# Kernel optimization log

Hardware: AMD Instinct MI355X
Metric: run time of the kernel (lower is better)

## Reference

```python
import jax, jax.numpy as jnp
import numpy as np

B, H, S, D = 4, 16, 2048, 64
TEMPERATURE = 8.0  # sqrt(D)
NEG = -1000000000.0

def setup_inputs() -> dict:
    key = jax.random.key(0)
    kq, kk, kv, km = jax.random.split(key, 4)
    q = jax.random.normal(kq, (B, H, S, D), dtype=jnp.float32)
    k = jax.random.normal(kk, (B, H, S, D), dtype=jnp.float32)
    v = jax.random.normal(kv, (B, H, S, D), dtype=jnp.float32)
    mask = jax.random.randint(km, (B, 1, S, S), 0, 2, dtype=jnp.int32)
    return {"q": q, "k": k, "v": v, "mask": mask}

def reference(q, k, v, mask):
    # scores: [B,H,S,S]
    scores = jnp.einsum('bhqd,bhkd->bhqk', q / TEMPERATURE, k)
    scores = jnp.where(mask == 1, NEG, scores)
    attn = jax.nn.softmax(scores, axis=-1)  # dropout p=0.0 -> identity
    out = jnp.einsum('bhqk,bhkd->bhqd', attn, v)
    return out
```

## Files before the change

kernel.cpp:

```cpp
#include <hip/hip_runtime.h>

#define NB 4
#define NH 16
#define SS 2048
#define DD 64
#define QT 256
#define KT 64
#define NT (SS / KT)
#define KSP 72
#define QSCALE 0.18033688011112042f

#define WS_BITS_BYTES ((size_t)NB * SS * (SS / 8))
#define WS_KB_OFF  ((size_t)2  << 20)
#define WS_VB_OFF  ((size_t)18 << 20)
#define WS_FULL    ((size_t)34 << 20)

typedef __bf16 bf16x8 __attribute__((ext_vector_type(8)));
typedef __bf16 bf16x2 __attribute__((ext_vector_type(2)));
typedef float  floatx16 __attribute__((ext_vector_type(16)));
typedef unsigned long long u64t;

static_assert(sizeof(bf16x8) == 16, "bf16x8 must be 16B");

__device__ __forceinline__ int pack2(float a, float b) {
    bf16x2 v; v[0] = (__bf16)a; v[1] = (__bf16)b;
    return __builtin_bit_cast(int, v);
}

__device__ __forceinline__ int vperm_col(int k) {
    return 16 * (k >> 4) + 8 * ((k >> 2) & 1) + (k & 3) + 4 * ((k >> 3) & 1);
}
__device__ __forceinline__ int vperm_inv(int c) {
    return 16 * ((c >> 4) & 3) + 8 * ((c >> 2) & 1) + 4 * ((c >> 3) & 1) + (c & 3);
}

__global__ __launch_bounds__(256)
void pack_mask_kernel(const int* __restrict__ M, u64t* __restrict__ bits)
{
    const int w    = (blockIdx.x * 256 + threadIdx.x) >> 6;
    const int lane = threadIdx.x & 63;
    #pragma unroll 4
    for (int i = 0; i < 16; ++i) {
        const int gw   = i * 16384 + w;
        const size_t row = (size_t)(gw >> 5);
        const int word = gw & 31;
        const int mval = M[row * SS + (size_t)word * 64 + lane];
        const u64t b = __ballot(mval == 1);
        if (lane == 0) bits[gw] = b;
    }
}

__global__ __launch_bounds__(256)
void pre_kernel(const float* __restrict__ K, const float* __restrict__ V,
                const int* __restrict__ M, u64t* __restrict__ bits,
                __bf16* __restrict__ KB, __bf16* __restrict__ VB)
{
    __shared__ float vt[64][68];
    const int t = threadIdx.x;

    if (blockIdx.x < 2048) {
        const int bh = blockIdx.x >> 5;
        const int tt = blockIdx.x & 31;
        const size_t tb = (size_t)bh * SS * DD + (size_t)tt * (KT * DD);

        {
            const float* src = K + tb + t * 16;
            __bf16* dst = KB + tb + t * 16;
            float4 f0 = ((const float4*)src)[0];
            float4 f1 = ((const float4*)src)[1];
            float4 f2 = ((const float4*)src)[2];
            float4 f3 = ((const float4*)src)[3];
            bf16x8 o0, o1;
            o0[0]=(__bf16)f0.x; o0[1]=(__bf16)f0.y; o0[2]=(__bf16)f0.z; o0[3]=(__bf16)f0.w;
            o0[4]=(__bf16)f1.x; o0[5]=(__bf16)f1.y; o0[6]=(__bf16)f1.z; o0[7]=(__bf16)f1.w;
            o1[0]=(__bf16)f2.x; o1[1]=(__bf16)f2.y; o1[2]=(__bf16)f2.z; o1[3]=(__bf16)f2.w;
            o1[4]=(__bf16)f3.x; o1[5]=(__bf16)f3.y; o1[6]=(__bf16)f3.z; o1[7]=(__bf16)f3.w;
            ((bf16x8*)dst)[0] = o0;
            ((bf16x8*)dst)[1] = o1;
        }

        {
            const int key = t >> 2, ds = (t & 3) * 16;
            const float* src = V + tb + (size_t)key * DD + ds;
            #pragma unroll
            for (int i = 0; i < 4; ++i)
                *(float4*)&vt[key][ds + 4 * i] = ((const float4*)src)[i];
        }
        __syncthreads();
        {
            const int dim = t >> 2, cb = (t & 3) * 16;
            bf16x8 o0, o1;
            #pragma unroll
            for (int c = 0; c < 16; ++c) {
                const float vvv = vt[vperm_inv(cb + c)][dim];
                if (c < 8) o0[c] = (__bf16)vvv; else o1[c - 8] = (__bf16)vvv;
            }
            __bf16* dst = VB + tb + (size_t)dim * 64 + cb;
            ((bf16x8*)dst)[0] = o0;
            ((bf16x8*)dst)[1] = o1;
        }
    } else {
        const int w    = ((blockIdx.x - 2048) * 256 + t) >> 6;
        const int lane = t & 63;
        #pragma unroll 4
        for (int i = 0; i < 16; ++i) {
            const int gw   = i * 16384 + w;
            const size_t row = (size_t)(gw >> 5);
            const int word = gw & 31;
            const int mval = M[row * SS + (size_t)word * 64 + lane];
            const u64t b = __ballot(mval == 1);
            if (lane == 0) bits[gw] = b;
        }
    }
}

__global__ __launch_bounds__(256, 2)
void attn2_kernel(const float* __restrict__ Q, const unsigned* __restrict__ MBu,
                  const __bf16* __restrict__ KB, const __bf16* __restrict__ VB,
                  float* __restrict__ O)
{
    __shared__ __bf16 ks [2][KT][KSP];
    __shared__ __bf16 vsT[2][DD][KSP];

    const int t    = threadIdx.x;
    const int lane = t & 63;
    const int l31  = lane & 31;
    const int h8   = lane >> 5;
    const int wave = t >> 6;

    const int bh    = blockIdx.x & 63;
    const int qtile = blockIdx.x >> 6;
    const int b     = bh >> 4;
    const int q0    = qtile * QT + wave * 64;

    const size_t base = (size_t)bh * SS * DD;

    bf16x8 aqA[4], aqB[4];
    #pragma unroll
    for (int grp = 0; grp < 2; ++grp) {
        const float* qp = Q + base + (size_t)(q0 + 32 * grp + l31) * DD + 8 * h8;
        #pragma unroll
        for (int s = 0; s < 4; ++s) {
            float4 f0 = *(const float4*)(qp + 16 * s);
            float4 f1 = *(const float4*)(qp + 16 * s + 4);
            bf16x8 a;
            a[0] = (__bf16)(f0.x * QSCALE); a[1] = (__bf16)(f0.y * QSCALE);
            a[2] = (__bf16)(f0.z * QSCALE); a[3] = (__bf16)(f0.w * QSCALE);
            a[4] = (__bf16)(f1.x * QSCALE); a[5] = (__bf16)(f1.y * QSCALE);
            a[6] = (__bf16)(f1.z * QSCALE); a[7] = (__bf16)(f1.w * QSCALE);
            if (grp == 0) aqA[s] = a; else aqB[s] = a;
        }
    }

    const int srow = t >> 3;
    const int sc8  = (t & 7) * 8;
    const __bf16* kbp = KB + base + (size_t)srow * DD + sc8;
    const __bf16* vbp = VB + base + (size_t)srow * DD + sc8;
    bf16x8 kr0, kr1, vr0, vr1;

    kr0 = *(const bf16x8*)kbp;
    kr1 = *(const bf16x8*)(kbp + 32 * DD);
    vr0 = *(const bf16x8*)vbp;
    vr1 = *(const bf16x8*)(vbp + 32 * DD);

    const u64t* mbrA = (const u64t*)MBu + ((size_t)b * SS + q0 + l31)      * (SS / 64);
    const u64t* mbrB = (const u64t*)MBu + ((size_t)b * SS + q0 + 32 + l31) * (SS / 64);
    u64t mA = mbrA[0], mB = mbrB[0], mnA, mnB;

    floatx16 o0A, o1A, o0B, o1B;
    #pragma unroll
    for (int i = 0; i < 16; ++i) {
        o0A[i] = 0.f; o1A[i] = 0.f; o0B[i] = 0.f; o1B[i] = 0.f;
    }
    float lsA = 0.f, lsB = 0.f;

    for (int tt = 0; tt < NT; ++tt) {
        const int cur = tt & 1;

        *(bf16x8*)&ks [cur][srow]     [sc8] = kr0;
        *(bf16x8*)&ks [cur][srow + 32][sc8] = kr1;
        *(bf16x8*)&vsT[cur][srow]     [sc8] = vr0;
        *(bf16x8*)&vsT[cur][srow + 32][sc8] = vr1;

        asm volatile("s_waitcnt lgkmcnt(0)" ::: "memory");
        __builtin_amdgcn_s_barrier();
        asm volatile("" ::: "memory");

        {
            const size_t jn = (size_t)((tt + 1) & (NT - 1)) * (KT * DD);
            kr0 = *(const bf16x8*)(kbp + jn);
            kr1 = *(const bf16x8*)(kbp + jn + 32 * DD);
            vr0 = *(const bf16x8*)(vbp + jn);
            vr1 = *(const bf16x8*)(vbp + jn + 32 * DD);
        }
        mnA = mbrA[(tt + 1) & (NT - 1)];
        mnB = mbrB[(tt + 1) & (NT - 1)];

        __builtin_amdgcn_s_setprio(1);

        bf16x8 kf0[4], kf1[4];
        #pragma unroll
        for (int s = 0; s < 4; ++s) {
            kf0[s] = *(const bf16x8*)&ks[cur][l31]     [16 * s + 8 * h8];
            kf1[s] = *(const bf16x8*)&ks[cur][32 + l31][16 * s + 8 * h8];
        }

        floatx16 cA0, cB0, cA1, cB1;
        {
            const unsigned uA0 = (unsigned)(mA)       >> (4 * h8);
            const unsigned uB0 = (unsigned)(mB)       >> (4 * h8);
            const unsigned uA1 = (unsigned)(mA >> 32) >> (4 * h8);
            const unsigned uB1 = (unsigned)(mB >> 32) >> (4 * h8);
            #pragma unroll
            for (int i = 0; i < 16; ++i) {
                const int pos = (i & 3) + 8 * (i >> 2);
                cA0[i] = __builtin_bit_cast(float, (((int)(uA0 << (31 - pos))) >> 31) & (int)0xC4800000u);
                cB0[i] = __builtin_bit_cast(float, (((int)(uB0 << (31 - pos))) >> 31) & (int)0xC4800000u);
                cA1[i] = __builtin_bit_cast(float, (((int)(uA1 << (31 - pos))) >> 31) & (int)0xC4800000u);
                cB1[i] = __builtin_bit_cast(float, (((int)(uB1 << (31 - pos))) >> 31) & (int)0xC4800000u);
            }
        }

        #pragma unroll
        for (int s = 0; s < 4; ++s) {
            cA0 = __builtin_amdgcn_mfma_f32_32x32x16_bf16(kf0[s], aqA[s], cA0, 0, 0, 0);
            cB0 = __builtin_amdgcn_mfma_f32_32x32x16_bf16(kf0[s], aqB[s], cB0, 0, 0, 0);
            cA1 = __builtin_amdgcn_mfma_f32_32x32x16_bf16(kf1[s], aqA[s], cA1, 0, 0, 0);
            cB1 = __builtin_amdgcn_mfma_f32_32x32x16_bf16(kf1[s], aqB[s], cB1, 0, 0, 0);
        }

        int pkA0[8], pkB0[8];
        {
            float sa0 = 0.f, sa1 = 0.f, sb0 = 0.f, sb1 = 0.f;
            #pragma unroll
            for (int g = 0; g < 8; ++g) {
                float a0 = __builtin_amdgcn_exp2f(cA0[2 * g]);
                float a1 = __builtin_amdgcn_exp2f(cA0[2 * g + 1]);
                float b0 = __builtin_amdgcn_exp2f(cB0[2 * g]);
                float b1 = __builtin_amdgcn_exp2f(cB0[2 * g + 1]);
                sa0 += a0; sa1 += a1; sb0 += b0; sb1 += b1;
                pkA0[g] = pack2(a0, a1);
                pkB0[g] = pack2(b0, b1);
            }
            lsA += sa0 + sa1; lsB += sb0 + sb1;
        }

        #pragma unroll
        for (int s2 = 0; s2 < 2; ++s2) {
            bf16x8 av0 = *(const bf16x8*)&vsT[cur][l31]     [16 * s2 + 8 * h8];
            bf16x8 av1 = *(const bf16x8*)&vsT[cur][32 + l31][16 * s2 + 8 * h8];
            int4 fwA; fwA.x = pkA0[4*s2]; fwA.y = pkA0[4*s2+1]; fwA.z = pkA0[4*s2+2]; fwA.w = pkA0[4*s2+3];
            int4 fwB; fwB.x = pkB0[4*s2]; fwB.y = pkB0[4*s2+1]; fwB.z = pkB0[4*s2+2]; fwB.w = pkB0[4*s2+3];
            bf16x8 bpA = __builtin_bit_cast(bf16x8, fwA);
            bf16x8 bpB = __builtin_bit_cast(bf16x8, fwB);
            o0A = __builtin_amdgcn_mfma_f32_32x32x16_bf16(av0, bpA, o0A, 0, 0, 0);
            o0B = __builtin_amdgcn_mfma_f32_32x32x16_bf16(av0, bpB, o0B, 0, 0, 0);
            o1A = __builtin_amdgcn_mfma_f32_32x32x16_bf16(av1, bpA, o1A, 0, 0, 0);
            o1B = __builtin_amdgcn_mfma_f32_32x32x16_bf16(av1, bpB, o1B, 0, 0, 0);
        }

        int pkA1[8], pkB1[8];
        {
            float sa0 = 0.f, sa1 = 0.f, sb0 = 0.f, sb1 = 0.f;
            #pragma unroll
            for (int g = 0; g < 8; ++g) {
                float a0 = __builtin_amdgcn_exp2f(cA1[2 * g]);
                float a1 = __builtin_amdgcn_exp2f(cA1[2 * g + 1]);
                float b0 = __builtin_amdgcn_exp2f(cB1[2 * g]);
                float b1 = __builtin_amdgcn_exp2f(cB1[2 * g + 1]);
                sa0 += a0; sa1 += a1; sb0 += b0; sb1 += b1;
                pkA1[g] = pack2(a0, a1);
                pkB1[g] = pack2(b0, b1);
            }
            lsA += sa0 + sa1; lsB += sb0 + sb1;
        }

        #pragma unroll
        for (int s2 = 0; s2 < 2; ++s2) {
            bf16x8 av0 = *(const bf16x8*)&vsT[cur][l31]     [32 + 16 * s2 + 8 * h8];
            bf16x8 av1 = *(const bf16x8*)&vsT[cur][32 + l31][32 + 16 * s2 + 8 * h8];
            int4 fwA; fwA.x = pkA1[4*s2]; fwA.y = pkA1[4*s2+1]; fwA.z = pkA1[4*s2+2]; fwA.w = pkA1[4*s2+3];
            int4 fwB; fwB.x = pkB1[4*s2]; fwB.y = pkB1[4*s2+1]; fwB.z = pkB1[4*s2+2]; fwB.w = pkB1[4*s2+3];
            bf16x8 bpA = __builtin_bit_cast(bf16x8, fwA);
            bf16x8 bpB = __builtin_bit_cast(bf16x8, fwB);
            o0A = __builtin_amdgcn_mfma_f32_32x32x16_bf16(av0, bpA, o0A, 0, 0, 0);
            o0B = __builtin_amdgcn_mfma_f32_32x32x16_bf16(av0, bpB, o0B, 0, 0, 0);
            o1A = __builtin_amdgcn_mfma_f32_32x32x16_bf16(av1, bpA, o1A, 0, 0, 0);
            o1B = __builtin_amdgcn_mfma_f32_32x32x16_bf16(av1, bpB, o1B, 0, 0, 0);
        }

        __builtin_amdgcn_s_setprio(0);

        mA = mnA; mB = mnB;
    }

    lsA += __shfl_xor(lsA, 32);
    lsB += __shfl_xor(lsB, 32);
    const float invA = 1.0f / lsA;
    const float invB = 1.0f / lsB;
    float* opA = O + base + (size_t)(q0 + l31) * DD;
    float* opB = O + base + (size_t)(q0 + 32 + l31) * DD;
    #pragma unroll
    for (int s = 0; s < 4; ++s) {
        float4 st;
        st.x = o0A[4*s+0] * invA; st.y = o0A[4*s+1] * invA;
        st.z = o0A[4*s+2] * invA; st.w = o0A[4*s+3] * invA;
        *(float4*)(opA + 8 * s + 4 * h8) = st;
        st.x = o1A[4*s+0] * invA; st.y = o1A[4*s+1] * invA;
        st.z = o1A[4*s+2] * invA; st.w = o1A[4*s+3] * invA;
        *(float4*)(opA + 32 + 8 * s + 4 * h8) = st;
        st.x = o0B[4*s+0] * invB; st.y = o0B[4*s+1] * invB;
        st.z = o0B[4*s+2] * invB; st.w = o0B[4*s+3] * invB;
        *(float4*)(opB + 8 * s + 4 * h8) = st;
        st.x = o1B[4*s+0] * invB; st.y = o1B[4*s+1] * invB;
        st.z = o1B[4*s+2] * invB; st.w = o1B[4*s+3] * invB;
        *(float4*)(opB + 32 + 8 * s + 4 * h8) = st;
    }
}

template<int MODE>
__global__ __launch_bounds__(512, 4)
void attn_kernel(const float* __restrict__ Q, const float* __restrict__ K,
                 const float* __restrict__ V, const int* __restrict__ M,
                 const unsigned* __restrict__ MB, float* __restrict__ O)
{
    __shared__ __bf16 ks [2][KT][KSP];
    __shared__ __bf16 vsT[2][DD][KSP];

    const int t    = threadIdx.x;
    const int wave = t >> 6;
    const int lane = t & 63;
    const int l31  = lane & 31;
    const int h8   = lane >> 5;

    const int bh    = blockIdx.x & 63;
    const int qtile = blockIdx.x >> 6;
    const int b     = bh >> 4;
    const int q0    = qtile * QT + wave * 32;

    const size_t base = (size_t)bh * SS * DD;

    bf16x8 aq[4];
    {
        const float* qp = Q + base + (size_t)(q0 + l31) * DD + 8 * h8;
        #pragma unroll
        for (int s = 0; s < 4; ++s) {
            float4 f0 = *(const float4*)(qp + 16 * s);
            float4 f1 = *(const float4*)(qp + 16 * s + 4);
            bf16x8 a;
            a[0] = (__bf16)(f0.x * QSCALE); a[1] = (__bf16)(f0.y * QSCALE);
            a[2] = (__bf16)(f0.z * QSCALE); a[3] = (__bf16)(f0.w * QSCALE);
            a[4] = (__bf16)(f1.x * QSCALE); a[5] = (__bf16)(f1.y * QSCALE);
            a[6] = (__bf16)(f1.z * QSCALE); a[7] = (__bf16)(f1.w * QSCALE);
            aq[s] = a;
        }
    }

    bf16x8 ones8;
    #pragma unroll
    for (int i = 0; i < 8; ++i) ones8[i] = (__bf16)1.0f;

    const int skey = t >> 3;
    const int sdc  = (t & 7) * 8;
    const int vk   = 2 * (t & 31);
    const int vdc  = (t >> 5) * 4;
    const int vcol = vperm_col(vk);
    const float* kp0 = K + base + (size_t)skey * DD + sdc;
    const float* vp0 = V + base + (size_t)vk * DD + vdc;

    float4 ka0 = ((const float4*)kp0)[0];
    float4 ka1 = ((const float4*)kp0)[1];
    float4 va0 = *(const float4*)(vp0);
    float4 va1 = *(const float4*)(vp0 + DD);

    const u64t* mbrow = (const u64t*)MB + ((size_t)b * SS + q0 + l31) * (SS / 64);
    const int*  mrow  = M + (size_t)b * SS * SS + (size_t)(q0 + l31) * SS + 4 * h8;
    u64t mall = 0, mnext = 0;
    if constexpr (MODE >= 1) mall = mbrow[0];

    floatx16 o0, o1, oL;
    #pragma unroll
    for (int i = 0; i < 16; ++i) { o0[i] = 0.f; o1[i] = 0.f; oL[i] = 0.f; }

    for (int tt = 0; tt < NT; ++tt) {
        const int cur = tt & 1;

        {
            bf16x8 kw;
            kw[0]=(__bf16)ka0.x; kw[1]=(__bf16)ka0.y; kw[2]=(__bf16)ka0.z; kw[3]=(__bf16)ka0.w;
            kw[4]=(__bf16)ka1.x; kw[5]=(__bf16)ka1.y; kw[6]=(__bf16)ka1.z; kw[7]=(__bf16)ka1.w;
            *(bf16x8*)&ks[cur][skey][sdc] = kw;
            #pragma unroll
            for (int i = 0; i < 4; ++i) {
                bf16x2 pr;
                pr[0] = (__bf16)(&va0.x)[i]; pr[1] = (__bf16)(&va1.x)[i];
                *(bf16x2*)&vsT[cur][vdc + i][vcol] = pr;
            }
        }
        __syncthreads();

        int4 mi[8];
        if constexpr (MODE == 0) {
            #pragma unroll
            for (int g = 0; g < 8; ++g)
                mi[g] = *(const int4*)(mrow + tt * KT + 8 * g);
        }

        {
            const int jn = ((tt + 1) * KT) & (SS - 1);
            const float* kn = kp0 + (size_t)jn * DD;
            ka0 = ((const float4*)kn)[0];
            ka1 = ((const float4*)kn)[1];
            const float* vn = vp0 + (size_t)jn * DD;
            va0 = *(const float4*)(vn);
            va1 = *(const float4*)(vn + DD);
        }
        if constexpr (MODE >= 1) mnext = mbrow[(tt + 1) & (NT - 1)];

        #pragma unroll
        for (int half = 0; half < 2; ++half) {
            floatx16 c;
            if constexpr (MODE >= 1) {
                const unsigned u = (unsigned)(mall >> (32 * half)) >> (4 * h8);
                #pragma unroll
                for (int i = 0; i < 16; ++i) {
                    const int pos = (i & 3) + 8 * (i >> 2);
                    const int sm = ((int)(u << (31 - pos))) >> 31;
                    c[i] = __builtin_bit_cast(float, sm & (int)0xC4800000u);
                }
            } else {
                #pragma unroll
                for (int i = 0; i < 16; ++i) {
                    const int g2 = 4 * half + (i >> 2);
                    c[i] = ((&mi[g2].x)[i & 3] == 1) ? -1024.0f : 0.0f;
                }
            }

            __builtin_amdgcn_s_setprio(1);
            #pragma unroll
            for (int s = 0; s < 4; ++s) {
                bf16x8 a = *(const bf16x8*)&ks[cur][32 * half + l31][16 * s + 8 * h8];
                c = __builtin_amdgcn_mfma_f32_32x32x16_bf16(a, aq[s], c, 0, 0, 0);
            }
            __builtin_amdgcn_s_setprio(0);

            int pk[8];
            #pragma unroll
            for (int g = 0; g < 8; ++g) {
                float pa = __builtin_amdgcn_exp2f(c[2 * g]);
                float pb = __builtin_amdgcn_exp2f(c[2 * g + 1]);
                pk[g] = pack2(pa, pb);
            }

            __builtin_amdgcn_s_setprio(1);
            #pragma unroll
            for (int s2 = 0; s2 < 2; ++s2) {
                int4 fw; fw.x = pk[4*s2]; fw.y = pk[4*s2+1]; fw.z = pk[4*s2+2]; fw.w = pk[4*s2+3];
                bf16x8 bp = __builtin_bit_cast(bf16x8, fw);
                bf16x8 av0 = *(const bf16x8*)&vsT[cur][l31]     [32 * half + 16 * s2 + 8 * h8];
                bf16x8 av1 = *(const bf16x8*)&vsT[cur][32 + l31][32 * half + 16 * s2 + 8 * h8];
                o0 = __builtin_amdgcn_mfma_f32_32x32x16_bf16(av0, bp, o0, 0, 0, 0);
                o1 = __builtin_amdgcn_mfma_f32_32x32x16_bf16(av1, bp, o1, 0, 0, 0);
                oL = __builtin_amdgcn_mfma_f32_32x32x16_bf16(ones8, bp, oL, 0, 0, 0);
            }
            __builtin_amdgcn_s_setprio(0);
        }

        if constexpr (MODE >= 1) mall = mnext;
    }

    float inv = 1.0f / oL[0];
    float* op = O + base + (size_t)(q0 + l31) * DD;
    #pragma unroll
    for (int s = 0; s < 4; ++s) {
        float4 st0, st1;
        st0.x = o0[4*s+0] * inv; st0.y = o0[4*s+1] * inv;
        st0.z = o0[4*s+2] * inv; st0.w = o0[4*s+3] * inv;
        st1.x = o1[4*s+0] * inv; st1.y = o1[4*s+1] * inv;
        st1.z = o1[4*s+2] * inv; st1.w = o1[4*s+3] * inv;
        *(float4*)(op + 8 * s + 4 * h8)      = st0;
        *(float4*)(op + 32 + 8 * s + 4 * h8) = st1;
    }
}

extern "C" void kernel_launch(void* const* d_in, const int* in_sizes, int n_in,
                              void* d_out, int out_size, void* d_ws, size_t ws_size,
                              hipStream_t stream) {
    (void)in_sizes; (void)n_in; (void)out_size;
    const float* q = (const float*)d_in[0];
    const float* k = (const float*)d_in[1];
    const float* v = (const float*)d_in[2];
    const int*   m = (const int*)d_in[3];
    float* out = (float*)d_out;
    dim3 grid(NB * NH * (SS / QT));

    if (ws_size >= WS_FULL) {
        u64t*   bits = (u64t*)d_ws;
        __bf16* kb16 = (__bf16*)((char*)d_ws + WS_KB_OFF);
        __bf16* vb16 = (__bf16*)((char*)d_ws + WS_VB_OFF);
        pre_kernel<<<dim3(6144), 256, 0, stream>>>(k, v, m, bits, kb16, vb16);
        attn2_kernel<<<grid, 256, 0, stream>>>(q, (const unsigned*)bits,
                                               kb16, vb16, out);
    } else if (ws_size >= WS_BITS_BYTES) {
        u64t* bits = (u64t*)d_ws;
        pack_mask_kernel<<<dim3(4096), 256, 0, stream>>>(m, bits);
        attn_kernel<1><<<grid, 512, 0, stream>>>(q, k, v, m, (const unsigned*)bits, out);
    } else {
        attn_kernel<0><<<grid, 512, 0, stream>>>(q, k, v, m, nullptr, out);
    }
}
```

Baseline: 270.1 us.

## Pre-swizzle K/V into MFMA fragment order and load directly to registers, dropping LDS

```diff
diff --git a/kernel.cpp b/kernel.cpp
--- a/kernel.cpp
+++ b/kernel.cpp
@@ -55,7 +55,7 @@
                 const int* __restrict__ M, u64t* __restrict__ bits,
                 __bf16* __restrict__ KB, __bf16* __restrict__ VB)
 {
-    __shared__ float vt[64][68];
+    __shared__ float ft[64][68];
     const int t = threadIdx.x;
 
     if (blockIdx.x < 2048) {
@@ -64,40 +64,49 @@
         const size_t tb = (size_t)bh * SS * DD + (size_t)tt * (KT * DD);
 
         {
-            const float* src = K + tb + t * 16;
-            __bf16* dst = KB + tb + t * 16;
-            float4 f0 = ((const float4*)src)[0];
-            float4 f1 = ((const float4*)src)[1];
-            float4 f2 = ((const float4*)src)[2];
-            float4 f3 = ((const float4*)src)[3];
-            bf16x8 o0, o1;
-            o0[0]=(__bf16)f0.x; o0[1]=(__bf16)f0.y; o0[2]=(__bf16)f0.z; o0[3]=(__bf16)f0.w;
-            o0[4]=(__bf16)f1.x; o0[5]=(__bf16)f1.y; o0[6]=(__bf16)f1.z; o0[7]=(__bf16)f1.w;
-            o1[0]=(__bf16)f2.x; o1[1]=(__bf16)f2.y; o1[2]=(__bf16)f2.z; o1[3]=(__bf16)f2.w;
-            o1[4]=(__bf16)f3.x; o1[5]=(__bf16)f3.y; o1[6]=(__bf16)f3.z; o1[7]=(__bf16)f3.w;
-            ((bf16x8*)dst)[0] = o0;
-            ((bf16x8*)dst)[1] = o1;
-        }
+            const int key = t >> 2, ds = (t & 3) * 16;
+            const float* src = K + tb + (size_t)key * DD + ds;
+            #pragma unroll
+            for (int i = 0; i < 4; ++i)
+                *(float4*)&ft[key][ds + 4 * i] = ((const float4*)src)[i];
+        }
+        __syncthreads();
+        {
+            #pragma unroll
+            for (int rep = 0; rep < 2; ++rep) {
+                const int s = t + 256 * rep;
+                const int c = s >> 6, l = s & 63;
+                const int row = 32 * (c >> 2) + (l & 31);
+                const int col = 16 * (c & 3) + 8 * (l >> 5);
+                bf16x8 o;
+                #pragma unroll
+                for (int j = 0; j < 8; ++j) o[j] = (__bf16)ft[row][col + j];
+                *(bf16x8*)(KB + tb + (size_t)s * 8) = o;
+            }
+        }
+        __syncthreads();
 
         {
             const int key = t >> 2, ds = (t & 3) * 16;
             const float* src = V + tb + (size_t)key * DD + ds;
             #pragma unroll
             for (int i = 0; i < 4; ++i)
-                *(float4*)&vt[key][ds + 4 * i] = ((const float4*)src)[i];
+                *(float4*)&ft[key][ds + 4 * i] = ((const float4*)src)[i];
         }
         __syncthreads();
         {
-            const int dim = t >> 2, cb = (t & 3) * 16;
-            bf16x8 o0, o1;
-            #pragma unroll
-            for (int c = 0; c < 16; ++c) {
-                const float vvv = vt[vperm_inv(cb + c)][dim];
-                if (c < 8) o0[c] = (__bf16)vvv; else o1[c - 8] = (__bf16)vvv;
-            }
-            __bf16* dst = VB + tb + (size_t)dim * 64 + cb;
-            ((bf16x8*)dst)[0] = o0;
-            ((bf16x8*)dst)[1] = o1;
+            #pragma unroll
+            for (int rep = 0; rep < 2; ++rep) {
+                const int s = t + 256 * rep;
+                const int g = s >> 6, l = s & 63;
+                const int colb = 32 * (g >> 2) + 16 * ((g >> 1) & 1) + 8 * (l >> 5);
+                const int dim  = 32 * (g & 1) + (l & 31);
+                bf16x8 o;
+                #pragma unroll
+                for (int j = 0; j < 8; ++j)
+                    o[j] = (__bf16)ft[vperm_inv(colb + j)][dim];
+                *(bf16x8*)(VB + tb + (size_t)s * 8) = o;
+            }
         }
     } else {
         const int w    = ((blockIdx.x - 2048) * 256 + t) >> 6;
@@ -116,12 +125,9 @@
 
 __global__ __launch_bounds__(256, 2)
 void attn2_kernel(const float* __restrict__ Q, const unsigned* __restrict__ MBu,
-                  const __bf16* __restrict__ KB, const __bf16* __restrict__ VB,
+                  const __bf16* __restrict__ KBf, const __bf16* __restrict__ VBf,
                   float* __restrict__ O)
 {
-    __shared__ __bf16 ks [2][KT][KSP];
-    __shared__ __bf16 vsT[2][DD][KSP];
-
     const int t    = threadIdx.x;
     const int lane = t & 63;
     const int l31  = lane & 31;
@@ -152,20 +158,18 @@
         }
     }
 
-    const int srow = t >> 3;
-    const int sc8  = (t & 7) * 8;
-    const __bf16* kbp = KB + base + (size_t)srow * DD + sc8;
-    const __bf16* vbp = VB + base + (size_t)srow * DD + sc8;
-    bf16x8 kr0, kr1, vr0, vr1;
-
-    kr0 = *(const bf16x8*)kbp;
-    kr1 = *(const bf16x8*)(kbp + 32 * DD);
-    vr0 = *(const bf16x8*)vbp;
-    vr1 = *(const bf16x8*)(vbp + 32 * DD);
+    const __bf16* kfp = KBf + base + (size_t)lane * 8;
+    const __bf16* vfp = VBf + base + (size_t)lane * 8;
+
+    bf16x8 kf[8], vfr[8];
+    #pragma unroll
+    for (int g = 0; g < 8; ++g) kf[g]  = *(const bf16x8*)(kfp + g * 512);
+    #pragma unroll
+    for (int g = 0; g < 8; ++g) vfr[g] = *(const bf16x8*)(vfp + g * 512);
 
     const u64t* mbrA = (const u64t*)MBu + ((size_t)b * SS + q0 + l31)      * (SS / 64);
     const u64t* mbrB = (const u64t*)MBu + ((size_t)b * SS + q0 + 32 + l31) * (SS / 64);
-    u64t mA = mbrA[0], mB = mbrB[0], mnA, mnB;
+    u64t mA = mbrA[0], mB = mbrB[0];
 
     floatx16 o0A, o1A, o0B, o1B;
     #pragma unroll
@@ -175,35 +179,7 @@
     float lsA = 0.f, lsB = 0.f;
 
     for (int tt = 0; tt < NT; ++tt) {
-        const int cur = tt & 1;
-
-        *(bf16x8*)&ks [cur][srow]     [sc8] = kr0;
-        *(bf16x8*)&ks [cur][srow + 32][sc8] = kr1;
-        *(bf16x8*)&vsT[cur][srow]     [sc8] = vr0;
-        *(bf16x8*)&vsT[cur][srow + 32][sc8] = vr1;
-
-        asm volatile("s_waitcnt lgkmcnt(0)" ::: "memory");
-        __builtin_amdgcn_s_barrier();
-        asm volatile("" ::: "memory");
-
-        {
-            const size_t jn = (size_t)((tt + 1) & (NT - 1)) * (KT * DD);
-            kr0 = *(const bf16x8*)(kbp + jn);
-            kr1 = *(const bf16x8*)(kbp + jn + 32 * DD);
-            vr0 = *(const bf16x8*)(vbp + jn);
-            vr1 = *(const bf16x8*)(vbp + jn + 32 * DD);
-        }
-        mnA = mbrA[(tt + 1) & (NT - 1)];
-        mnB = mbrB[(tt + 1) & (NT - 1)];
-
-        __builtin_amdgcn_s_setprio(1);
-
-        bf16x8 kf0[4], kf1[4];
-        #pragma unroll
-        for (int s = 0; s < 4; ++s) {
-            kf0[s] = *(const bf16x8*)&ks[cur][l31]     [16 * s + 8 * h8];
-            kf1[s] = *(const bf16x8*)&ks[cur][32 + l31][16 * s + 8 * h8];
-        }
+        const size_t jn = (size_t)((tt + 1) & (NT - 1)) * (KT * DD);
 
         floatx16 cA0, cB0, cA1, cB1;
         {
@@ -220,14 +196,22 @@
                 cB1[i] = __builtin_bit_cast(float, (((int)(uB1 << (31 - pos))) >> 31) & (int)0xC4800000u);
             }
         }
-
+        mA = mbrA[(tt + 1) & (NT - 1)];
+        mB = mbrB[(tt + 1) & (NT - 1)];
+
+        __builtin_amdgcn_s_setprio(1);
         #pragma unroll
         for (int s = 0; s < 4; ++s) {
-            cA0 = __builtin_amdgcn_mfma_f32_32x32x16_bf16(kf0[s], aqA[s], cA0, 0, 0, 0);
-            cB0 = __builtin_amdgcn_mfma_f32_32x32x16_bf16(kf0[s], aqB[s], cB0, 0, 0, 0);
-            cA1 = __builtin_amdgcn_mfma_f32_32x32x16_bf16(kf1[s], aqA[s], cA1, 0, 0, 0);
-            cB1 = __builtin_amdgcn_mfma_f32_32x32x16_bf16(kf1[s], aqB[s], cB1, 0, 0, 0);
-        }
+            cA0 = __builtin_amdgcn_mfma_f32_32x32x16_bf16(kf[s],     aqA[s], cA0, 0, 0, 0);
+            cB0 = __builtin_amdgcn_mfma_f32_32x32x16_bf16(kf[s],     aqB[s], cB0, 0, 0, 0);
+            cA1 = __builtin_amdgcn_mfma_f32_32x32x16_bf16(kf[4 + s], aqA[s], cA1, 0, 0, 0);
+            cB1 = __builtin_amdgcn_mfma_f32_32x32x16_bf16(kf[4 + s], aqB[s], cB1, 0, 0, 0);
+        }
+        __builtin_amdgcn_s_setprio(0);
+
+        #pragma unroll
+        for (int g = 0; g < 8; ++g)
+            kf[g] = *(const bf16x8*)(kfp + jn + g * 512);
 
         int pkA0[8], pkB0[8];
         {
@@ -245,10 +229,11 @@
             lsA += sa0 + sa1; lsB += sb0 + sb1;
         }
 
+        __builtin_amdgcn_s_setprio(1);
         #pragma unroll
         for (int s2 = 0; s2 < 2; ++s2) {
-            bf16x8 av0 = *(const bf16x8*)&vsT[cur][l31]     [16 * s2 + 8 * h8];
-            bf16x8 av1 = *(const bf16x8*)&vsT[cur][32 + l31][16 * s2 + 8 * h8];
+            bf16x8 av0 = vfr[s2 * 2 + 0];
+            bf16x8 av1 = vfr[s2 * 2 + 1];
             int4 fwA; fwA.x = pkA0[4*s2]; fwA.y = pkA0[4*s2+1]; fwA.z = pkA0[4*s2+2]; fwA.w = pkA0[4*s2+3];
             int4 fwB; fwB.x = pkB0[4*s2]; fwB.y = pkB0[4*s2+1]; fwB.z = pkB0[4*s2+2]; fwB.w = pkB0[4*s2+3];
             bf16x8 bpA = __builtin_bit_cast(bf16x8, fwA);
@@ -258,6 +243,7 @@
             o1A = __builtin_amdgcn_mfma_f32_32x32x16_bf16(av1, bpA, o1A, 0, 0, 0);
             o1B = __builtin_amdgcn_mfma_f32_32x32x16_bf16(av1, bpB, o1B, 0, 0, 0);
         }
+        __builtin_amdgcn_s_setprio(0);
 
         int pkA1[8], pkB1[8];
         {
@@ -275,10 +261,11 @@
             lsA += sa0 + sa1; lsB += sb0 + sb1;
         }
 
+        __builtin_amdgcn_s_setprio(1);
         #pragma unroll
         for (int s2 = 0; s2 < 2; ++s2) {
-            bf16x8 av0 = *(const bf16x8*)&vsT[cur][l31]     [32 + 16 * s2 + 8 * h8];
-            bf16x8 av1 = *(const bf16x8*)&vsT[cur][32 + l31][32 + 16 * s2 + 8 * h8];
+            bf16x8 av0 = vfr[4 + s2 * 2 + 0];
+            bf16x8 av1 = vfr[4 + s2 * 2 + 1];
             int4 fwA; fwA.x = pkA1[4*s2]; fwA.y = pkA1[4*s2+1]; fwA.z = pkA1[4*s2+2]; fwA.w = pkA1[4*s2+3];
             int4 fwB; fwB.x = pkB1[4*s2]; fwB.y = pkB1[4*s2+1]; fwB.z = pkB1[4*s2+2]; fwB.w = pkB1[4*s2+3];
             bf16x8 bpA = __builtin_bit_cast(bf16x8, fwA);
@@ -288,10 +275,11 @@
             o1A = __builtin_amdgcn_mfma_f32_32x32x16_bf16(av1, bpA, o1A, 0, 0, 0);
             o1B = __builtin_amdgcn_mfma_f32_32x32x16_bf16(av1, bpB, o1B, 0, 0, 0);
         }
-
         __builtin_amdgcn_s_setprio(0);
 
-        mA = mnA; mB = mnB;
+        #pragma unroll
+        for (int g = 0; g < 8; ++g)
+            vfr[g] = *(const bf16x8*)(vfp + jn + g * 512);
     }
 
     lsA += __shfl_xor(lsA, 32);
```

New measurement: 303.6 us. +12.4%, slower.

## Double the key tile per barrier stage to 128 keys in attention kernel

Applied to the files above, without the earlier changes.

```diff
diff --git a/kernel.cpp b/kernel.cpp
--- a/kernel.cpp
+++ b/kernel.cpp
@@ -6,8 +6,10 @@
 #define DD 64
 #define QT 256
 #define KT 64
-#define NT (SS / KT)
+#define ST 128
+#define NST (SS / ST)
 #define KSP 72
+#define VSP 136
 #define QSCALE 0.18033688011112042f
 
 #define WS_BITS_BYTES ((size_t)NB * SS * (SS / 8))
@@ -119,8 +121,8 @@
                   const __bf16* __restrict__ KB, const __bf16* __restrict__ VB,
                   float* __restrict__ O)
 {
-    __shared__ __bf16 ks [2][KT][KSP];
-    __shared__ __bf16 vsT[2][DD][KSP];
+    __shared__ __bf16 ks [2][ST][KSP];
+    __shared__ __bf16 vsT[2][DD][VSP];
 
     const int t    = threadIdx.x;
     const int lane = t & 63;
@@ -156,16 +158,21 @@
     const int sc8  = (t & 7) * 8;
     const __bf16* kbp = KB + base + (size_t)srow * DD + sc8;
     const __bf16* vbp = VB + base + (size_t)srow * DD + sc8;
-    bf16x8 kr0, kr1, vr0, vr1;
-
-    kr0 = *(const bf16x8*)kbp;
-    kr1 = *(const bf16x8*)(kbp + 32 * DD);
-    vr0 = *(const bf16x8*)vbp;
-    vr1 = *(const bf16x8*)(vbp + 32 * DD);
+    bf16x8 kr[4], vr[4];
+
+    {
+        #pragma unroll
+        for (int i = 0; i < 4; ++i)
+            kr[i] = *(const bf16x8*)(kbp + (size_t)(32 * i) * DD);
+        vr[0] = *(const bf16x8*)(vbp);
+        vr[1] = *(const bf16x8*)(vbp + 32 * DD);
+        vr[2] = *(const bf16x8*)(vbp + KT * DD);
+        vr[3] = *(const bf16x8*)(vbp + KT * DD + 32 * DD);
+    }
 
     const u64t* mbrA = (const u64t*)MBu + ((size_t)b * SS + q0 + l31)      * (SS / 64);
     const u64t* mbrB = (const u64t*)MBu + ((size_t)b * SS + q0 + 32 + l31) * (SS / 64);
-    u64t mA = mbrA[0], mB = mbrB[0], mnA, mnB;
+    u64t mA0 = mbrA[0], mA1 = mbrA[1], mB0 = mbrB[0], mB1 = mbrB[1];
 
     floatx16 o0A, o1A, o0B, o1B;
     #pragma unroll
@@ -174,124 +181,139 @@
     }
     float lsA = 0.f, lsB = 0.f;
 
-    for (int tt = 0; tt < NT; ++tt) {
+    for (int tt = 0; tt < NST; ++tt) {
         const int cur = tt & 1;
 
-        *(bf16x8*)&ks [cur][srow]     [sc8] = kr0;
-        *(bf16x8*)&ks [cur][srow + 32][sc8] = kr1;
-        *(bf16x8*)&vsT[cur][srow]     [sc8] = vr0;
-        *(bf16x8*)&vsT[cur][srow + 32][sc8] = vr1;
+        #pragma unroll
+        for (int i = 0; i < 4; ++i)
+            *(bf16x8*)&ks[cur][srow + 32 * i][sc8] = kr[i];
+        *(bf16x8*)&vsT[cur][srow]     [sc8]      = vr[0];
+        *(bf16x8*)&vsT[cur][srow + 32][sc8]      = vr[1];
+        *(bf16x8*)&vsT[cur][srow]     [64 + sc8] = vr[2];
+        *(bf16x8*)&vsT[cur][srow + 32][64 + sc8] = vr[3];
 
         asm volatile("s_waitcnt lgkmcnt(0)" ::: "memory");
         __builtin_amdgcn_s_barrier();
         asm volatile("" ::: "memory");
 
         {
-            const size_t jn = (size_t)((tt + 1) & (NT - 1)) * (KT * DD);
-            kr0 = *(const bf16x8*)(kbp + jn);
-            kr1 = *(const bf16x8*)(kbp + jn + 32 * DD);
-            vr0 = *(const bf16x8*)(vbp + jn);
-            vr1 = *(const bf16x8*)(vbp + jn + 32 * DD);
-        }
-        mnA = mbrA[(tt + 1) & (NT - 1)];
-        mnB = mbrB[(tt + 1) & (NT - 1)];
-
-        __builtin_amdgcn_s_setprio(1);
-
-        bf16x8 kf0[4], kf1[4];
+            const size_t jn = (size_t)((tt + 1) & (NST - 1)) * (ST * DD);
+            #pragma unroll
+            for (int i = 0; i < 4; ++i)
+                kr[i] = *(const bf16x8*)(kbp + jn + (size_t)(32 * i) * DD);
+            vr[0] = *(const bf16x8*)(vbp + jn);
+            vr[1] = *(const bf16x8*)(vbp + jn + 32 * DD);
+            vr[2] = *(const bf16x8*)(vbp + jn + KT * DD);
+            vr[3] = *(const bf16x8*)(vbp + jn + KT * DD + 32 * DD);
+        }
+        const int nw = (2 * tt + 2) & (2 * NST - 1);
+        u64t nA0 = mbrA[nw], nA1 = mbrA[nw + 1];
+        u64t nB0 = mbrB[nw], nB1 = mbrB[nw + 1];
+
         #pragma unroll
-        for (int s = 0; s < 4; ++s) {
-            kf0[s] = *(const bf16x8*)&ks[cur][l31]     [16 * s + 8 * h8];
-            kf1[s] = *(const bf16x8*)&ks[cur][32 + l31][16 * s + 8 * h8];
-        }
-
-        floatx16 cA0, cB0, cA1, cB1;
-        {
-            const unsigned uA0 = (unsigned)(mA)       >> (4 * h8);
-            const unsigned uB0 = (unsigned)(mB)       >> (4 * h8);
-            const unsigned uA1 = (unsigned)(mA >> 32) >> (4 * h8);
-            const unsigned uB1 = (unsigned)(mB >> 32) >> (4 * h8);
-            #pragma unroll
-            for (int i = 0; i < 16; ++i) {
-                const int pos = (i & 3) + 8 * (i >> 2);
-                cA0[i] = __builtin_bit_cast(float, (((int)(uA0 << (31 - pos))) >> 31) & (int)0xC4800000u);
-                cB0[i] = __builtin_bit_cast(float, (((int)(uB0 << (31 - pos))) >> 31) & (int)0xC4800000u);
-                cA1[i] = __builtin_bit_cast(float, (((int)(uA1 << (31 - pos))) >> 31) & (int)0xC4800000u);
-                cB1[i] = __builtin_bit_cast(float, (((int)(uB1 << (31 - pos))) >> 31) & (int)0xC4800000u);
-            }
-        }
-
-        #pragma unroll
-        for (int s = 0; s < 4; ++s) {
-            cA0 = __builtin_amdgcn_mfma_f32_32x32x16_bf16(kf0[s], aqA[s], cA0, 0, 0, 0);
-            cB0 = __builtin_amdgcn_mfma_f32_32x32x16_bf16(kf0[s], aqB[s], cB0, 0, 0, 0);
-            cA1 = __builtin_amdgcn_mfma_f32_32x32x16_bf16(kf1[s], aqA[s], cA1, 0, 0, 0);
-            cB1 = __builtin_amdgcn_mfma_f32_32x32x16_bf16(kf1[s], aqB[s], cB1, 0, 0, 0);
-        }
-
-        int pkA0[8], pkB0[8];
-        {
-            float sa0 = 0.f, sa1 = 0.f, sb0 = 0.f, sb1 = 0.f;
-            #pragma unroll
-            for (int g = 0; g < 8; ++g) {
-                float a0 = __builtin_amdgcn_exp2f(cA0[2 * g]);
-                float a1 = __builtin_amdgcn_exp2f(cA0[2 * g + 1]);
-                float b0 = __builtin_amdgcn_exp2f(cB0[2 * g]);
-                float b1 = __builtin_amdgcn_exp2f(cB0[2 * g + 1]);
-                sa0 += a0; sa1 += a1; sb0 += b0; sb1 += b1;
-                pkA0[g] = pack2(a0, a1);
-                pkB0[g] = pack2(b0, b1);
-            }
-            lsA += sa0 + sa1; lsB += sb0 + sb1;
-        }
-
-        #pragma unroll
-        for (int s2 = 0; s2 < 2; ++s2) {
-            bf16x8 av0 = *(const bf16x8*)&vsT[cur][l31]     [16 * s2 + 8 * h8];
-            bf16x8 av1 = *(const bf16x8*)&vsT[cur][32 + l31][16 * s2 + 8 * h8];
-            int4 fwA; fwA.x = pkA0[4*s2]; fwA.y = pkA0[4*s2+1]; fwA.z = pkA0[4*s2+2]; fwA.w = pkA0[4*s2+3];
-            int4 fwB; fwB.x = pkB0[4*s2]; fwB.y = pkB0[4*s2+1]; fwB.z = pkB0[4*s2+2]; fwB.w = pkB0[4*s2+3];
-            bf16x8 bpA = __builtin_bit_cast(bf16x8, fwA);
-            bf16x8 bpB = __builtin_bit_cast(bf16x8, fwB);
-            o0A = __builtin_amdgcn_mfma_f32_32x32x16_bf16(av0, bpA, o0A, 0, 0, 0);
-            o0B = __builtin_amdgcn_mfma_f32_32x32x16_bf16(av0, bpB, o0B, 0, 0, 0);
-            o1A = __builtin_amdgcn_mfma_f32_32x32x16_bf16(av1, bpA, o1A, 0, 0, 0);
-            o1B = __builtin_amdgcn_mfma_f32_32x32x16_bf16(av1, bpB, o1B, 0, 0, 0);
-        }
-
-        int pkA1[8], pkB1[8];
-        {
-            float sa0 = 0.f, sa1 = 0.f, sb0 = 0.f, sb1 = 0.f;
-            #pragma unroll
-            for (int g = 0; g < 8; ++g) {
-                float a0 = __builtin_amdgcn_exp2f(cA1[2 * g]);
-                float a1 = __builtin_amdgcn_exp2f(cA1[2 * g + 1]);
-                float b0 = __builtin_amdgcn_exp2f(cB1[2 * g]);
-                float b1 = __builtin_amdgcn_exp2f(cB1[2 * g + 1]);
-                sa0 += a0; sa1 += a1; sb0 += b0; sb1 += b1;
-                pkA1[g] = pack2(a0, a1);
-                pkB1[g] = pack2(b0, b1);
-            }
-            lsA += sa0 + sa1; lsB += sb0 + sb1;
-        }
-
-        #pragma unroll
-        for (int s2 = 0; s2 < 2; ++s2) {
-            bf16x8 av0 = *(const bf16x8*)&vsT[cur][l31]     [32 + 16 * s2 + 8 * h8];
-            bf16x8 av1 = *(const bf16x8*)&vsT[cur][32 + l31][32 + 16 * s2 + 8 * h8];
-            int4 fwA; fwA.x = pkA1[4*s2]; fwA.y = pkA1[4*s2+1]; fwA.z = pkA1[4*s2+2]; fwA.w = pkA1[4*s2+3];
-            int4 fwB; fwB.x = pkB1[4*s2]; fwB.y = pkB1[4*s2+1]; fwB.z = pkB1[4*s2+2]; fwB.w = pkB1[4*s2+3];
-            bf16x8 bpA = __builtin_bit_cast(bf16x8, fwA);
-            bf16x8 bpB = __builtin_bit_cast(bf16x8, fwB);
-            o0A = __builtin_amdgcn_mfma_f32_32x32x16_bf16(av0, bpA, o0A, 0, 0, 0);
-            o0B = __builtin_amdgcn_mfma_f32_32x32x16_bf16(av0, bpB, o0B, 0, 0, 0);
-            o1A = __builtin_amdgcn_mfma_f32_32x32x16_bf16(av1, bpA, o1A, 0, 0, 0);
-            o1B = __builtin_amdgcn_mfma_f32_32x32x16_bf16(av1, bpB, o1B, 0, 0, 0);
-        }
-
-        __builtin_amdgcn_s_setprio(0);
-
-        mA = mnA; mB = mnB;
+        for (int hp = 0; hp < 2; ++hp) {
+            const u64t wA = hp ? mA1 : mA0;
+            const u64t wB = hp ? mB1 : mB0;
+
+            floatx16 cA0, cB0, cA1, cB1;
+            {
+                const unsigned uA0 = (unsigned)(wA)       >> (4 * h8);
+                const unsigned uB0 = (unsigned)(wB)       >> (4 * h8);
+                const unsigned uA1 = (unsigned)(wA >> 32) >> (4 * h8);
+                const unsigned uB1 = (unsigned)(wB >> 32) >> (4 * h8);
+                #pragma unroll
+                for (int i = 0; i < 16; ++i) {
+                    const int pos = (i & 3) + 8 * (i >> 2);
+                    cA0[i] = __builtin_bit_cast(float, (((int)(uA0 << (31 - pos))) >> 31) & (int)0xC4800000u);
+                    cB0[i] = __builtin_bit_cast(float, (((int)(uB0 << (31 - pos))) >> 31) & (int)0xC4800000u);
+                    cA1[i] = __builtin_bit_cast(float, (((int)(uA1 << (31 - pos))) >> 31) & (int)0xC4800000u);
+                    cB1[i] = __builtin_bit_cast(float, (((int)(uB1 << (31 - pos))) >> 31) & (int)0xC4800000u);
+                }
+            }
+
+            __builtin_amdgcn_s_setprio(1);
+            bf16x8 kf0[4], kf1[4];
+            #pragma unroll
+            for (int s = 0; s < 4; ++s) {
+                kf0[s] = *(const bf16x8*)&ks[cur][64 * hp + l31]     [16 * s + 8 * h8];
+                kf1[s] = *(const bf16x8*)&ks[cur][64 * hp + 32 + l31][16 * s + 8 * h8];
+            }
+
+            #pragma unroll
+            for (int s = 0; s < 4; ++s) {
+                cA0 = __builtin_amdgcn_mfma_f32_32x32x16_bf16(kf0[s], aqA[s], cA0, 0, 0, 0);
+                cB0 = __builtin_amdgcn_mfma_f32_32x32x16_bf16(kf0[s], aqB[s], cB0, 0, 0, 0);
+                cA1 = __builtin_amdgcn_mfma_f32_32x32x16_bf16(kf1[s], aqA[s], cA1, 0, 0, 0);
+                cB1 = __builtin_amdgcn_mfma_f32_32x32x16_bf16(kf1[s], aqB[s], cB1, 0, 0, 0);
+            }
+            __builtin_amdgcn_s_setprio(0);
+
+            int pkA0[8], pkB0[8];
+            {
+                float sa0 = 0.f, sa1 = 0.f, sb0 = 0.f, sb1 = 0.f;
+                #pragma unroll
+                for (int g = 0; g < 8; ++g) {
+                    float a0 = __builtin_amdgcn_exp2f(cA0[2 * g]);
+                    float a1 = __builtin_amdgcn_exp2f(cA0[2 * g + 1]);
+                    float b0 = __builtin_amdgcn_exp2f(cB0[2 * g]);
+                    float b1 = __builtin_amdgcn_exp2f(cB0[2 * g + 1]);
+                    sa0 += a0; sa1 += a1; sb0 += b0; sb1 += b1;
+                    pkA0[g] = pack2(a0, a1);
+                    pkB0[g] = pack2(b0, b1);
+                }
+                lsA += sa0 + sa1; lsB += sb0 + sb1;
+            }
+
+            __builtin_amdgcn_s_setprio(1);
+            #pragma unroll
+            for (int s2 = 0; s2 < 2; ++s2) {
+                bf16x8 av0 = *(const bf16x8*)&vsT[cur][l31]     [64 * hp + 16 * s2 + 8 * h8];
+                bf16x8 av1 = *(const bf16x8*)&vsT[cur][32 + l31][64 * hp + 16 * s2 + 8 * h8];
+                int4 fwA; fwA.x = pkA0[4*s2]; fwA.y = pkA0[4*s2+1]; fwA.z = pkA0[4*s2+2]; fwA.w = pkA0[4*s2+3];
+                int4 fwB; fwB.x = pkB0[4*s2]; fwB.y = pkB0[4*s2+1]; fwB.z = pkB0[4*s2+2]; fwB.w = pkB0[4*s2+3];
+                bf16x8 bpA = __builtin_bit_cast(bf16x8, fwA);
+                bf16x8 bpB = __builtin_bit_cast(bf16x8, fwB);
+                o0A = __builtin_amdgcn_mfma_f32_32x32x16_bf16(av0, bpA, o0A, 0, 0, 0);
+                o0B = __builtin_amdgcn_mfma_f32_32x32x16_bf16(av0, bpB, o0B, 0, 0, 0);
+                o1A = __builtin_amdgcn_mfma_f32_32x32x16_bf16(av1, bpA, o1A, 0, 0, 0);
+                o1B = __builtin_amdgcn_mfma_f32_32x32x16_bf16(av1, bpB, o1B, 0, 0, 0);
+            }
+            __builtin_amdgcn_s_setprio(0);
+
+            int pkA1[8], pkB1[8];
+            {
+                float sa0 = 0.f, sa1 = 0.f, sb0 = 0.f, sb1 = 0.f;
+                #pragma unroll
+                for (int g = 0; g < 8; ++g) {
+                    float a0 = __builtin_amdgcn_exp2f(cA1[2 * g]);
+                    float a1 = __builtin_amdgcn_exp2f(cA1[2 * g + 1]);
+                    float b0 = __builtin_amdgcn_exp2f(cB1[2 * g]);
+                    float b1 = __builtin_amdgcn_exp2f(cB1[2 * g + 1]);
+                    sa0 += a0; sa1 += a1; sb0 += b0; sb1 += b1;
+                    pkA1[g] = pack2(a0, a1);
+                    pkB1[g] = pack2(b0, b1);
+                }
+                lsA += sa0 + sa1; lsB += sb0 + sb1;
+            }
+
+            __builtin_amdgcn_s_setprio(1);
+            #pragma unroll
+            for (int s2 = 0; s2 < 2; ++s2) {
+                bf16x8 av0 = *(const bf16x8*)&vsT[cur][l31]     [64 * hp + 32 + 16 * s2 + 8 * h8];
+                bf16x8 av1 = *(const bf16x8*)&vsT[cur][32 + l31][64 * hp + 32 + 16 * s2 + 8 * h8];
+                int4 fwA; fwA.x = pkA1[4*s2]; fwA.y = pkA1[4*s2+1]; fwA.z = pkA1[4*s2+2]; fwA.w = pkA1[4*s2+3];
+                int4 fwB; fwB.x = pkB1[4*s2]; fwB.y = pkB1[4*s2+1]; fwB.z = pkB1[4*s2+2]; fwB.w = pkB1[4*s2+3];
+                bf16x8 bpA = __builtin_bit_cast(bf16x8, fwA);
+                bf16x8 bpB = __builtin_bit_cast(bf16x8, fwB);
+                o0A = __builtin_amdgcn_mfma_f32_32x32x16_bf16(av0, bpA, o0A, 0, 0, 0);
+                o0B = __builtin_amdgcn_mfma_f32_32x32x16_bf16(av0, bpB, o0B, 0, 0, 0);
+                o1A = __builtin_amdgcn_mfma_f32_32x32x16_bf16(av1, bpA, o1A, 0, 0, 0);
+                o1B = __builtin_amdgcn_mfma_f32_32x32x16_bf16(av1, bpB, o1B, 0, 0, 0);
+            }
+            __builtin_amdgcn_s_setprio(0);
+        }
+
+        mA0 = nA0; mA1 = nA1; mB0 = nB0; mB1 = nB1;
     }
 
     lsA += __shfl_xor(lsA, 32);
@@ -382,7 +404,7 @@
     #pragma unroll
     for (int i = 0; i < 16; ++i) { o0[i] = 0.f; o1[i] = 0.f; oL[i] = 0.f; }
 
-    for (int tt = 0; tt < NT; ++tt) {
+    for (int tt = 0; tt < SS / KT; ++tt) {
         const int cur = tt & 1;
 
         {
@@ -415,7 +437,7 @@
             va0 = *(const float4*)(vn);
             va1 = *(const float4*)(vn + DD);
         }
-        if constexpr (MODE >= 1) mnext = mbrow[(tt + 1) & (NT - 1)];
+        if constexpr (MODE >= 1) mnext = mbrow[(tt + 1) & (SS / KT - 1)];
 
         #pragma unroll
         for (int half = 0; half < 2; ++half) {
```

After: 379.5 us. 40.5% more time.
